# Kernel tuning notes

Hardware: AMD Instinct MI355X
Metric: run time of the kernel (lower is better)

Reference implementation:

```python
import jax, jax.numpy as jnp
import numpy as np

NEG_INF = -jnp.inf


def conv2d(x, w, b, stride, pad):
    # x: [B,C,H,W], w: [O,I,kh,kw]
    y = jax.lax.conv_general_dilated(
        x, w, window_strides=(stride, stride),
        padding=[(pad, pad), (pad, pad)],
        dimension_numbers=('NCHW', 'OIHW', 'NCHW'))
    return y + b[None, :, None, None]


def maxpool3s2(x):
    return jax.lax.reduce_window(x, -jnp.inf, jax.lax.max,
                                 (1, 1, 3, 3), (1, 1, 2, 2), 'VALID')


def setup_inputs() -> dict:
    key = jax.random.key(0)
    ks = jax.random.split(key, 20)
    s = 0.02
    B, C, H, W = 64, 3, 224, 224
    D, HID, OUT, E = 9216, 288, 1000, 8   # feature_dim, hidden_dim, output_dim, n_experts
    GH = 72                               # gate hidden = hidden_dim // 4
    inp = {
        'x':   jax.random.normal(ks[0], (B, C, H, W), jnp.float32),
        'c1w': s * jax.random.normal(ks[1], (64, 3, 11, 11), jnp.float32),
        'c1b': jnp.zeros((64,), jnp.float32),
        'c2w': s * jax.random.normal(ks[2], (192, 64, 5, 5), jnp.float32),
        'c2b': jnp.zeros((192,), jnp.float32),
        'c3w': s * jax.random.normal(ks[3], (384, 192, 3, 3), jnp.float32),
        'c3b': jnp.zeros((384,), jnp.float32),
        'c4w': s * jax.random.normal(ks[4], (256, 384, 3, 3), jnp.float32),
        'c4b': jnp.zeros((256,), jnp.float32),
        'c5w': s * jax.random.normal(ks[5], (256, 256, 3, 3), jnp.float32),
        'c5b': jnp.zeros((256,), jnp.float32),
        'gw1': s * jax.random.normal(ks[6], (D, GH), jnp.float32),
        'gb1': jnp.zeros((GH,), jnp.float32),
        'gw2': s * jax.random.normal(ks[7], (GH, E), jnp.float32),
        'gb2': jnp.zeros((E,), jnp.float32),
        'ew1': s * jax.random.normal(ks[8], (E, D, HID), jnp.float32),
        'eb1': jnp.zeros((E, HID), jnp.float32),
        'ew2': s * jax.random.normal(ks[9], (E, HID, HID // 2), jnp.float32),
        'eb2': jnp.zeros((E, HID // 2), jnp.float32),
        'ew3': s * jax.random.normal(ks[10], (E, HID // 2, OUT), jnp.float32),
        'eb3': jnp.zeros((E, OUT), jnp.float32),
    }
    return inp


def reference(x, c1w, c1b, c2w, c2b, c3w, c3b, c4w, c4b, c5w, c5b,
              gw1, gb1, gw2, gb2, ew1, eb1, ew2, eb2, ew3, eb3):
    # ---- AlexNet-style feature extractor (224 branch) ----
    h = jax.nn.relu(conv2d(x, c1w, c1b, 4, 2))   # [B,64,55,55]
    h = maxpool3s2(h)                             # [B,64,27,27]
    h = jax.nn.relu(conv2d(h, c2w, c2b, 1, 2))   # [B,192,27,27]
    h = maxpool3s2(h)                             # [B,192,13,13]
    h = jax.nn.relu(conv2d(h, c3w, c3b, 1, 1))   # [B,384,13,13]
    h = jax.nn.relu(conv2d(h, c4w, c4b, 1, 1))   # [B,256,13,13]
    h = jax.nn.relu(conv2d(h, c5w, c5b, 1, 1))   # [B,256,13,13]
    h = maxpool3s2(h)                             # [B,256,6,6]
    # AdaptiveAvgPool2d((6,6)) on a 6x6 input is the identity.
    feat = h.reshape(h.shape[0], -1)              # [B,9216]

    # ---- Gate: top-2 routing (eval mode: no noise, no dropout) ----
    g = jax.nn.relu(feat @ gw1 + gb1)             # [B,72]
    logits = g @ gw2 + gb2                        # [B,8]
    topv, topi = jax.lax.top_k(logits, 2)         # [B,2]
    topw = jax.nn.softmax(topv, axis=-1)          # softmax over top-2 only
    B = logits.shape[0]
    gates = jnp.zeros_like(logits).at[jnp.arange(B)[:, None], topi].set(topw)  # [B,8]

    # ---- Dense per-expert 3-layer MLP over full batch (as in source) ----
    h1 = jax.nn.relu(jnp.einsum('bd,edh->ebh', feat, ew1) + eb1[:, None, :])   # [E,B,288]
    h2 = jax.nn.relu(jnp.einsum('ebh,ehk->ebk', h1, ew2) + eb2[:, None, :])    # [E,B,144]
    eo = jnp.einsum('ebk,eko->ebo', h2, ew3) + eb3[:, None, :]                 # [E,B,1000]
    # Weighted combine; gates are zero for non-top-2 experts, matching the
    # masked accumulation loop in the torch forward.
    out = jnp.einsum('ebo,be->bo', eo, gates)     # [B,1000]
    return out
```

## Files before the change

kernel.cpp:

```cpp
#include <hip/hip_runtime.h>
#include <math.h>

#define TPB 256

typedef short s16x8 __attribute__((ext_vector_type(8)));
typedef short s16x4 __attribute__((ext_vector_type(4)));
typedef float f32x4 __attribute__((ext_vector_type(4)));

__device__ inline void bsplit(float x, short& h, short& l){
  union { float f; unsigned u; } a, hf, rf;
  a.f = x;
  unsigned hu = (a.u + 0x7FFFu + ((a.u >> 16) & 1u)) >> 16;
  h = (short)hu;
  hf.u = hu << 16;
  rf.f = x - hf.f;
  l = (short)((rf.u + 0x7FFFu + ((rf.u >> 16) & 1u)) >> 16);
}
__device__ inline float b2f(short s){
  union { unsigned u; float f; } x;
  x.u = ((unsigned)(unsigned short)s) << 16;
  return x.f;
}

__global__ __launch_bounds__(TPB) void wsplit_k(
    const float* __restrict__ w, short* __restrict__ wh, short* __restrict__ wl,
    int C, int O, int ntap, int total)
{
  int idx = blockIdx.x*TPB + threadIdx.x;
  if (idx >= total) return;
  int c   = idx % C;
  int t2  = idx / C;
  int oc  = t2 % O;
  int tap = t2 / O;
  float x = w[((size_t)oc*C + c)*ntap + tap];
  short h, l; bsplit(x, h, l);
  int tile = oc >> 4, ln = oc & 15;
  int S    = ntap*(C >> 5);
  int sl   = tap*(C >> 5) + (c >> 5);
  int lg   = (c >> 3) & 3, j = c & 7;
  size_t dst = (((size_t)tile*S + sl)*64 + lg*16 + ln)*8 + j;
  wh[dst] = h; wl[dst] = l;
}

__global__ __launch_bounds__(TPB) void wsplit1_k(
    const float* __restrict__ w, short* __restrict__ wh, short* __restrict__ wl)
{
  int idx = blockIdx.x*TPB + threadIdx.x;
  if (idx >= 64*576) return;
  int k  = idx % 576;
  int oc = idx / 576;
  int g  = k >> 4, kw = k & 15;
  int c  = g / 12, kh = g % 12;
  float x = 0.f;
  if (kh < 11 && kw < 11)
    x = w[((size_t)oc*3 + c)*121 + kh*11 + kw];
  short h, l; bsplit(x, h, l);
  int m = oc >> 4, ln = oc & 15;
  int s = k >> 5, r = k & 31;
  int lg = r >> 3, j = r & 7;
  size_t dst = (((size_t)m*18 + s)*64 + lg*16 + ln)*8 + j;
  wh[dst] = h; wl[dst] = l;
}

__global__ __launch_bounds__(TPB) void wtrans_k(
    const float* __restrict__ w, float* __restrict__ wT, int K, int O)
{
  int idx = blockIdx.x*TPB + threadIdx.x;
  if (idx >= K*O) return;
  int oc = idx % O;
  int k  = idx / O;
  wT[idx] = w[(size_t)oc*K + k];
}

#define C1W 240
#define CV1_PL 33
__global__ __launch_bounds__(256, 2) void conv1m_k(
    const float* __restrict__ in, const short* __restrict__ whi,
    const short* __restrict__ wlo, const float* __restrict__ bias,
    short* __restrict__ yh, short* __restrict__ yl)
{
  __shared__ __align__(16) short lds[2][CV1_PL*C1W + 84];
  const int tid = threadIdx.x;
  const int oh = blockIdx.x % 55;
  const int b  = blockIdx.x / 55;
  const int nt = tid >> 6;
  const int ln = tid & 15;
  const int lg = (tid & 63) >> 4;
  const int lane = tid & 63;
  const int ow = nt*16 + ln;

  const float* ip = in + (size_t)b*3*224*224;
  for (int i = tid; i < CV1_PL*59; i += 256){
    int plane = i / 59;
    int p     = i % 59;
    int c = plane / 11, kh = plane % 11;
    int ih = oh*4 - 2 + kh;
    int col0 = p*4;
    const float* rowp = (ih >= 0 && ih < 224) ? ip + (size_t)c*50176 + (size_t)ih*224 : nullptr;
    short h[4], l[4];
    #pragma unroll
    for (int j=0;j<4;++j){
      int iw = col0 + j - 2;
      float v = (rowp && iw >= 0 && iw < 224) ? rowp[iw] : 0.f;
      bsplit(v, h[j], l[j]);
    }
    s16x4 hv = {h[0],h[1],h[2],h[3]}, lv = {l[0],l[1],l[2],l[3]};
    *reinterpret_cast<s16x4*>(&lds[0][plane*C1W + col0]) = hv;
    *reinterpret_cast<s16x4*>(&lds[1][plane*C1W + col0]) = lv;
  }
  __syncthreads();

  f32x4 acc[4];
  #pragma unroll
  for (int m=0;m<4;++m){
    const float4 bv = *reinterpret_cast<const float4*>(bias + m*16 + lg*4);
    acc[m] = (f32x4){bv.x, bv.y, bv.z, bv.w};
  }

  s16x8 ah[4], al[4], ahn[4], aln[4];
  #pragma unroll
  for (int m=0;m<4;++m){
    size_t ao = (((size_t)m*18 + 0)*64 + lane)*8;
    ah[m] = *reinterpret_cast<const s16x8*>(whi + ao);
    al[m] = *reinterpret_cast<const s16x8*>(wlo + ao);
  }

  #pragma unroll 1
  for (int s=0; s<18; ++s){
    if (s < 17){
      #pragma unroll
      for (int m=0;m<4;++m){
        size_t ao = (((size_t)m*18 + s + 1)*64 + lane)*8;
        ahn[m] = *reinterpret_cast<const s16x8*>(whi + ao);
        aln[m] = *reinterpret_cast<const s16x8*>(wlo + ao);
      }
    }
    int g  = 2*s + (lg >> 1);
    int c  = g / 12, kh = g % 12;
    int plane = c*11 + (kh < 11 ? kh : 10);
    int base  = plane*C1W + ow*4 + (lg & 1)*8;
    s16x4 h0 = *reinterpret_cast<const s16x4*>(&lds[0][base]);
    s16x4 h1 = *reinterpret_cast<const s16x4*>(&lds[0][base+4]);
    s16x4 l0 = *reinterpret_cast<const s16x4*>(&lds[1][base]);
    s16x4 l1 = *reinterpret_cast<const s16x4*>(&lds[1][base+4]);
    s16x8 bh = __builtin_shufflevector(h0, h1, 0,1,2,3,4,5,6,7);
    s16x8 bl = __builtin_shufflevector(l0, l1, 0,1,2,3,4,5,6,7);
    #pragma unroll
    for (int m=0;m<4;++m){
      acc[m] = __builtin_amdgcn_mfma_f32_16x16x32_bf16(al[m], bh, acc[m], 0,0,0);
      acc[m] = __builtin_amdgcn_mfma_f32_16x16x32_bf16(ah[m], bl, acc[m], 0,0,0);
      acc[m] = __builtin_amdgcn_mfma_f32_16x16x32_bf16(ah[m], bh, acc[m], 0,0,0);
    }
    #pragma unroll
    for (int m=0;m<4;++m){ ah[m] = ahn[m]; al[m] = aln[m]; }
  }

  if (ow < 55){
    size_t base = ((size_t)b*3025 + (size_t)oh*55 + ow)*64;
    #pragma unroll
    for (int m=0;m<4;++m){
      short h[4], l[4];
      #pragma unroll
      for (int r=0;r<4;++r) bsplit(fmaxf(acc[m][r], 0.f), h[r], l[r]);
      s16x4 hv = {h[0],h[1],h[2],h[3]}, lv = {l[0],l[1],l[2],l[3]};
      *reinterpret_cast<s16x4*>(yh + base + m*16 + lg*4) = hv;
      *reinterpret_cast<s16x4*>(yl + base + m*16 + lg*4) = lv;
    }
  }
}

__global__ __launch_bounds__(TPB) void pool1_k(
    const short* __restrict__ xh, const short* __restrict__ xl,
    short* __restrict__ yh, short* __restrict__ yl)
{
  int i = blockIdx.x*TPB + threadIdx.x;
  if (i >= 64*729*64) return;
  int c = i & 63;
  int t = i >> 6;
  int sp = t % 729;
  int b = t / 729;
  int r = sp/27, cc = sp%27;
  const short* ph = xh + (size_t)b*3025*64 + c;
  const short* pl = xl + (size_t)b*3025*64 + c;
  float m = -INFINITY;
  #pragma unroll
  for (int di=0;di<3;++di)
    #pragma unroll
    for (int dj=0;dj<3;++dj){
      size_t s = (size_t)((2*r+di)*55 + 2*cc+dj)*64;
      m = fmaxf(m, b2f(ph[s]) + b2f(pl[s]));
    }
  short h, l; bsplit(m, h, l);
  yh[i] = h; yl[i] = l;
}

__global__ __launch_bounds__(256, 2) void conv2m_k(
    const short* __restrict__ xh, const short* __restrict__ xl,
    const short* __restrict__ whi, const short* __restrict__ wlo,
    const float* __restrict__ bias, short* __restrict__ yh, short* __restrict__ yl)
{
  __shared__ __align__(16) short lds[2][217*72];
  const int tid = threadIdx.x;
  const int rg  = blockIdx.x;
  const int b   = blockIdx.y;
  const int wid = tid >> 6;
  const int ln  = tid & 15;
  const int lg  = (tid & 63) >> 4;
  const int lane = tid & 63;
  const int oc0 = wid*48;
  const int r0  = rg*3;

  int sb[6], nn[6];
  #pragma unroll
  for (int t=0;t<6;++t){
    int n = t*16 + ln;
    nn[t] = n;
    int ohl = n / 27, ow = n % 27;
    sb[t] = (n < 81) ? (ohl*31 + ow) : 0;
  }

  f32x4 acc[3][6];
  #pragma unroll
  for (int m=0;m<3;++m){
    const float4 bv = *reinterpret_cast<const float4*>(bias + oc0 + m*16 + lg*4);
    #pragma unroll
    for (int t=0;t<6;++t) acc[m][t] = (f32x4){bv.x, bv.y, bv.z, bv.w};
  }

  for (int i = tid; i < 217*8; i += 256){
    int sp = i >> 3, v = i & 7;
    int pr = sp/31, pc = sp%31;
    int ih = r0 - 2 + pr, iw = pc - 2;
    s16x8 hv = {0,0,0,0,0,0,0,0}, lv = {0,0,0,0,0,0,0,0};
    if (ih >= 0 && ih < 27 && iw >= 0 && iw < 27){
      size_t o = ((size_t)b*729 + ih*27 + iw)*64 + v*8;
      hv = *reinterpret_cast<const s16x8*>(xh + o);
      lv = *reinterpret_cast<const s16x8*>(xl + o);
    }
    *reinterpret_cast<s16x8*>(&lds[0][sp*72 + v*8]) = hv;
    *reinterpret_cast<s16x8*>(&lds[1][sp*72 + v*8]) = lv;
  }
  __syncthreads();

  #pragma unroll 1
  for (int tap=0; tap<25; ++tap){
    const int toff = (tap/5)*31 + (tap%5);
    #pragma unroll
    for (int h2=0; h2<2; ++h2){
      const size_t wo = (((size_t)(wid*3)*50 + tap*2 + h2)*64 + lane)*8;
      s16x8 ah0 = *reinterpret_cast<const s16x8*>(whi + wo);
      s16x8 ah1 = *reinterpret_cast<const s16x8*>(whi + wo + 25600);
      s16x8 ah2 = *reinterpret_cast<const s16x8*>(whi + wo + 51200);
      s16x8 al0 = *reinterpret_cast<const s16x8*>(wlo + wo);
      s16x8 al1 = *reinterpret_cast<const s16x8*>(wlo + wo + 25600);
      s16x8 al2 = *reinterpret_cast<const s16x8*>(wlo + wo + 51200);
      #pragma unroll
      for (int t=0;t<6;++t){
        int off = (sb[t] + toff)*72 + h2*32 + lg*8;
        s16x8 bh = *reinterpret_cast<const s16x8*>(&lds[0][off]);
        s16x8 bl = *reinterpret_cast<const s16x8*>(&lds[1][off]);
        acc[0][t] = __builtin_amdgcn_mfma_f32_16x16x32_bf16(al0, bh, acc[0][t], 0,0,0);
        acc[0][t] = __builtin_amdgcn_mfma_f32_16x16x32_bf16(ah0, bl, acc[0][t], 0,0,0);
        acc[0][t] = __builtin_amdgcn_mfma_f32_16x16x32_bf16(ah0, bh, acc[0][t], 0,0,0);
        acc[1][t] = __builtin_amdgcn_mfma_f32_16x16x32_bf16(al1, bh, acc[1][t], 0,0,0);
        acc[1][t] = __builtin_amdgcn_mfma_f32_16x16x32_bf16(ah1, bl, acc[1][t], 0,0,0);
        acc[1][t] = __builtin_amdgcn_mfma_f32_16x16x32_bf16(ah1, bh, acc[1][t], 0,0,0);
        acc[2][t] = __builtin_amdgcn_mfma_f32_16x16x32_bf16(al2, bh, acc[2][t], 0,0,0);
        acc[2][t] = __builtin_amdgcn_mfma_f32_16x16x32_bf16(ah2, bl, acc[2][t], 0,0,0);
        acc[2][t] = __builtin_amdgcn_mfma_f32_16x16x32_bf16(ah2, bh, acc[2][t], 0,0,0);
      }
    }
  }

  #pragma unroll
  for (int m=0;m<3;++m)
    #pragma unroll
    for (int t=0;t<6;++t){
      if (nn[t] < 81){
        int gsp = r0*27 + nn[t];
        size_t base = ((size_t)b*729 + gsp)*192 + oc0 + m*16 + lg*4;
        short h[4], l[4];
        #pragma unroll
        for (int r=0;r<4;++r) bsplit(fmaxf(acc[m][t][r], 0.f), h[r], l[r]);
        s16x4 hv = {h[0],h[1],h[2],h[3]}, lv = {l[0],l[1],l[2],l[3]};
        *reinterpret_cast<s16x4*>(yh + base) = hv;
        *reinterpret_cast<s16x4*>(yl + base) = lv;
      }
    }
}

__global__ __launch_bounds__(TPB) void pool2_k(
    const short* __restrict__ xh, const short* __restrict__ xl,
    short* __restrict__ yh, short* __restrict__ yl)
{
  int i = blockIdx.x*TPB + threadIdx.x;
  if (i >= 64*169*192) return;
  int c = i % 192;
  int t = i / 192;
  int sp = t % 169;
  int b = t / 169;
  int r = sp/13, cc = sp%13;
  const short* ph = xh + (size_t)b*729*192 + c;
  const short* pl = xl + (size_t)b*729*192 + c;
  float m = -INFINITY;
  #pragma unroll
  for (int di=0;di<3;++di)
    #pragma unroll
    for (int dj=0;dj<3;++dj){
      size_t s = (size_t)((2*r+di)*27 + 2*cc+dj)*192;
      m = fmaxf(m, b2f(ph[s]) + b2f(pl[s]));
    }
  short h, l; bsplit(m, h, l);
  yh[i] = h; yl[i] = l;
}

template<int C,int O>
__global__ __launch_bounds__(256, 3) void conv3m_k(
    const short* __restrict__ xh, const short* __restrict__ xl,
    const short* __restrict__ whi, const short* __restrict__ wlo,
    const float* __restrict__ bias, short* __restrict__ yh, short* __restrict__ yl)
{
  __shared__ __align__(16) short lds[2][225*40];
  const int tid = threadIdx.x;
  const int b   = blockIdx.y;
  const int wid = tid >> 6;
  const int ln  = tid & 15;
  const int lg  = (tid & 63) >> 4;
  const int lane = tid & 63;
  const int tileIdx = blockIdx.x*2 + (wid & 1);
  const int oc0 = tileIdx*16;
  const int ng  = wid >> 1;
  const int tbase  = ng ? 6 : 0;
  const int ntiles = ng ? 5 : 6;
  const int S3 = 9*(C/32);

  int sb[6], nn[6];
  #pragma unroll
  for (int t=0;t<6;++t){
    int n = (tbase + t)*16 + ln;
    nn[t] = n;
    int oh = n / 13, ow = n % 13;
    sb[t] = (n < 169) ? (oh*15 + ow) : 0;
  }

  f32x4 acc[6];
  const float4 bv = *reinterpret_cast<const float4*>(bias + oc0 + lg*4);
  #pragma unroll
  for (int t=0;t<6;++t) acc[t] = (f32x4){bv.x, bv.y, bv.z, bv.w};

  #pragma unroll 1
  for (int c0=0; c0<C; c0+=32){
    __syncthreads();
    for (int i = tid; i < 225*4; i += 256){
      int sp = i >> 2, v = i & 3;
      int r = sp/15, cc = sp%15;
      s16x8 hv = {0,0,0,0,0,0,0,0}, lv = {0,0,0,0,0,0,0,0};
      if (r >= 1 && r <= 13 && cc >= 1 && cc <= 13){
        size_t o = ((size_t)b*169 + (r-1)*13 + (cc-1))*C + c0 + v*8;
        hv = *reinterpret_cast<const s16x8*>(xh + o);
        lv = *reinterpret_cast<const s16x8*>(xl + o);
      }
      *reinterpret_cast<s16x8*>(&lds[0][sp*40 + v*8]) = hv;
      *reinterpret_cast<s16x8*>(&lds[1][sp*40 + v*8]) = lv;
    }
    __syncthreads();

    const size_t tb = (size_t)tileIdx*S3 + (c0 >> 5);
    s16x8 ah = *reinterpret_cast<const s16x8*>(whi + (tb*64 + lane)*8);
    s16x8 al = *reinterpret_cast<const s16x8*>(wlo + (tb*64 + lane)*8);
    #pragma unroll 1
    for (int tap=0; tap<9; ++tap){
      s16x8 ahn = ah, aln = al;
      if (tap < 8){
        size_t ao = ((tb + (size_t)(tap+1)*(C/32))*64 + lane)*8;
        ahn = *reinterpret_cast<const s16x8*>(whi + ao);
        aln = *reinterpret_cast<const s16x8*>(wlo + ao);
      }
      const int toff = (tap/3)*15 + (tap%3);
      #pragma unroll
      for (int t=0;t<6;++t){
        if (t < ntiles){
          int off = (sb[t] + toff)*40 + lg*8;
          s16x8 bh = *reinterpret_cast<const s16x8*>(&lds[0][off]);
          s16x8 bl = *reinterpret_cast<const s16x8*>(&lds[1][off]);
          acc[t] = __builtin_amdgcn_mfma_f32_16x16x32_bf16(al, bh, acc[t], 0,0,0);
          acc[t] = __builtin_amdgcn_mfma_f32_16x16x32_bf16(ah, bl, acc[t], 0,0,0);
          acc[t] = __builtin_amdgcn_mfma_f32_16x16x32_bf16(ah, bh, acc[t], 0,0,0);
        }
      }
      ah = ahn; al = aln;
    }
  }

  #pragma unroll
  for (int t=0;t<6;++t){
    if (t < ntiles && nn[t] < 169){
      size_t base = ((size_t)b*169 + nn[t])*O + oc0 + lg*4;
      short h[4], l[4];
      #pragma unroll
      for (int r=0;r<4;++r) bsplit(fmaxf(acc[t][r], 0.f), h[r], l[r]);
      s16x4 hv = {h[0],h[1],h[2],h[3]}, lv = {l[0],l[1],l[2],l[3]};
      *reinterpret_cast<s16x4*>(yh + base) = hv;
      *reinterpret_cast<s16x4*>(yl + base) = lv;
    }
  }
}

__global__ __launch_bounds__(TPB) void pool3_k(
    const short* __restrict__ xh, const short* __restrict__ xl,
    float* __restrict__ feat)
{
  int i = blockIdx.x*TPB + threadIdx.x;
  if (i >= 64*9216) return;
  int d = i % 9216;
  int b = i / 9216;
  int c = d / 36;
  int sp = d % 36;
  int r = sp/6, cc = sp%6;
  const short* ph = xh + (size_t)b*169*256 + c;
  const short* pl = xl + (size_t)b*169*256 + c;
  float m = -INFINITY;
  #pragma unroll
  for (int di=0;di<3;++di)
    #pragma unroll
    for (int dj=0;dj<3;++dj){
      size_t s = (size_t)((2*r+di)*13 + 2*cc+dj)*256;
      m = fmaxf(m, b2f(ph[s]) + b2f(pl[s]));
    }
  feat[i] = m;
}

__global__ __launch_bounds__(256) void gate1_k(
    const float* __restrict__ feat, const float* __restrict__ gw1T,
    const float* __restrict__ gb1, float* __restrict__ g)
{
  const int b    = blockIdx.x;
  const int h    = blockIdx.y*4 + (threadIdx.x >> 6);
  const int lane = threadIdx.x & 63;
  const float* f = feat + (size_t)b*9216;
  const float* w = gw1T + (size_t)h*9216;
  float s = 0.f;
  #pragma unroll
  for (int it=0; it<36; ++it){
    int d = it*256 + lane*4;
    float4 fv = *reinterpret_cast<const float4*>(f + d);
    float4 wv = *reinterpret_cast<const float4*>(w + d);
    s = fmaf(fv.x, wv.x, s);
    s = fmaf(fv.y, wv.y, s);
    s = fmaf(fv.z, wv.z, s);
    s = fmaf(fv.w, wv.w, s);
  }
  #pragma unroll
  for (int off=32; off; off>>=1) s += __shfl_down(s, off, 64);
  if (lane == 0) g[(size_t)b*72 + h] = fmaxf(s + gb1[h], 0.f);
}

__global__ __launch_bounds__(128) void gate2_k(
    const float* __restrict__ g, const float* __restrict__ gw2,
    const float* __restrict__ gb2, float* __restrict__ gates)
{
  const int b = blockIdx.x;
  const int tid = threadIdx.x;
  __shared__ float gs[72];
  __shared__ float logits[8];
  if (tid < 72) gs[tid] = g[(size_t)b*72 + tid];
  __syncthreads();
  if (tid < 8) {
    float acc = gb2[tid];
    for (int j=0;j<72;++j)
      acc = fmaf(gs[j], gw2[(size_t)j*8 + tid], acc);
    logits[tid] = acc;
  }
  __syncthreads();
  if (tid == 0) {
    int i1 = 0; float v1 = logits[0];
    for (int e=1;e<8;++e) if (logits[e] > v1) { v1 = logits[e]; i1 = e; }
    int i2 = -1; float v2 = -INFINITY;
    for (int e=0;e<8;++e) { if (e==i1) continue; if (logits[e] > v2) { v2 = logits[e]; i2 = e; } }
    float z  = expf(v2 - v1);
    float w1 = 1.f / (1.f + z);
    float w2 = z   / (1.f + z);
    float* gr = gates + (size_t)b*8;
    for (int e=0;e<8;++e) gr[e] = 0.f;
    gr[i1] = w1;
    gr[i2] = w2;
  }
}

__global__ __launch_bounds__(256, 2) void eh1_part_k(
    const float* __restrict__ feat, const float* __restrict__ ew1,
    float* __restrict__ part)
{
  const int e  = blockIdx.x;
  const int ks = blockIdx.y;
  const int nb = blockIdx.z;
  const int h0 = nb*144;
  __shared__ __align__(16) float fs[64*33];
  __shared__ __align__(16) float wsh[32*144];
  const int tid = threadIdx.x;
  const int tx = tid & 15;
  const int ty = tid >> 4;
  float acc[4][9];
  #pragma unroll
  for (int i=0;i<4;++i)
    #pragma unroll
    for (int j=0;j<9;++j) acc[i][j]=0.f;
  const float* wbase = ew1 + (size_t)e*9216*288 + h0;
  for (int d0 = ks*192; d0 < ks*192+192; d0 += 32){
    __syncthreads();
    for (int l = tid; l < 512; l += 256){
      int r = l >> 3, c = l & 7;
      float4 v = *reinterpret_cast<const float4*>(feat + (size_t)r*9216 + d0 + c*4);
      float* dst = &fs[r*33 + c*4];
      dst[0]=v.x; dst[1]=v.y; dst[2]=v.z; dst[3]=v.w;
    }
    for (int l = tid; l < 1152; l += 256){
      int r = l / 36, c = l % 36;
      *reinterpret_cast<float4*>(&wsh[r*144 + c*4]) =
        *reinterpret_cast<const float4*>(wbase + (size_t)(d0 + r)*288 + c*4);
    }
    __syncthreads();
    #pragma unroll
    for (int k=0;k<32;++k){
      float fv[4], wv[9];
      #pragma unroll
      for (int i=0;i<4;++i) fv[i] = fs[(ty*4+i)*33 + k];
      #pragma unroll
      for (int j=0;j<9;++j) wv[j] = wsh[k*144 + tx*9 + j];
      #pragma unroll
      for (int i=0;i<4;++i)
        #pragma unroll
        for (int j=0;j<9;++j)
          acc[i][j] = fmaf(fv[i], wv[j], acc[i][j]);
    }
  }
  float* pp = part + (size_t)(ks*8 + e)*64*288;
  #pragma unroll
  for (int i=0;i<4;++i)
    #pragma unroll
    for (int j=0;j<9;++j)
      pp[(ty*4+i)*288 + h0 + tx*9 + j] = acc[i][j];
}

__global__ __launch_bounds__(TPB) void eh1_reduce_k(
    const float* __restrict__ part, const float* __restrict__ eb1,
    float* __restrict__ h1)
{
  int idx = blockIdx.x*TPB + threadIdx.x;
  if (idx >= 8*64*288) return;
  int h = idx % 288;
  int e = idx / (64*288);
  float a = eb1[(size_t)e*288 + h];
  #pragma unroll
  for (int s=0;s<48;++s)
    a += part[(size_t)s*147456 + idx];
  h1[idx] = fmaxf(a, 0.f);
}

__global__ __launch_bounds__(TPB) void expert_h2_k(
    const float* __restrict__ h1, const float* __restrict__ ew2,
    const float* __restrict__ eb2, const float* __restrict__ gates,
    float* __restrict__ h2)
{
  int idx = blockIdx.x*TPB + threadIdx.x;
  if (idx >= 8*64*144) return;
  int k = idx % 144;
  int t = idx / 144;
  int b = t % 64;
  int e = t / 64;
  if (gates[(size_t)b*8 + e] == 0.f) return;
  float acc = eb2[(size_t)e*144 + k];
  const float* h = h1 + ((size_t)e*64 + b)*288;
  const float* w = ew2 + (size_t)e*288*144 + k;
  for (int d=0; d<288; ++d)
    acc = fmaf(h[d], w[(size_t)d*144], acc);
  h2[idx] = fmaxf(acc, 0.f);
}

__global__ __launch_bounds__(TPB) void expert_out_k(
    const float* __restrict__ h2, const float* __restrict__ ew3,
    const float* __restrict__ eb3, const float* __restrict__ gates,
    float* __restrict__ out)
{
  int idx = blockIdx.x*TPB + threadIdx.x;
  if (idx >= 64*1000) return;
  int o = idx % 1000;
  int b = idx / 1000;
  float acc = 0.f;
  const float* gr = gates + (size_t)b*8;
  for (int e=0;e<8;++e){
    float ge = gr[e];
    if (ge == 0.f) continue;
    float a = eb3[(size_t)e*1000 + o];
    const float* h = h2 + ((size_t)e*64 + b)*144;
    const float* w = ew3 + (size_t)e*144*1000 + o;
    for (int k=0;k<144;++k)
      a = fmaf(h[k], w[(size_t)k*1000], a);
    acc = fmaf(ge, a, acc);
  }
  out[idx] = acc;
}

static inline int nblk(long long n){ return (int)((n + TPB - 1) / TPB); }

extern "C" void kernel_launch(void* const* d_in, const int* in_sizes, int n_in,
                              void* d_out, int out_size, void* d_ws, size_t ws_size,
                              hipStream_t stream)
{
  const float* x   = (const float*)d_in[0];
  const float* c1w = (const float*)d_in[1];  const float* c1b = (const float*)d_in[2];
  const float* c2w = (const float*)d_in[3];  const float* c2b = (const float*)d_in[4];
  const float* c3w = (const float*)d_in[5];  const float* c3b = (const float*)d_in[6];
  const float* c4w = (const float*)d_in[7];  const float* c4b = (const float*)d_in[8];
  const float* c5w = (const float*)d_in[9];  const float* c5b = (const float*)d_in[10];
  const float* gw1 = (const float*)d_in[11]; const float* gb1 = (const float*)d_in[12];
  const float* gw2 = (const float*)d_in[13]; const float* gb2 = (const float*)d_in[14];
  const float* ew1 = (const float*)d_in[15]; const float* eb1 = (const float*)d_in[16];
  const float* ew2 = (const float*)d_in[17]; const float* eb2 = (const float*)d_in[18];
  const float* ew3 = (const float*)d_in[19]; const float* eb3 = (const float*)d_in[20];
  float* out = (float*)d_out;

  float* W = (float*)d_ws;
  short* X1H = (short*)W;
  short* X1L = X1H + 12390400;
  short* X3H = (short*)W;
  short* X3L = X3H + 8957952;
  short* X5H = (short*)W;
  short* X5L = X5H + 4153344;
  short* X7H = (short*)W;
  short* X7L = X7H + 2768896;
  float* feat  = W + 5000000;
  float* part  = W + 6000000;
  short* WH2 = (short*)(W +  9000000);
  short* WL2 = WH2 + 307200;
  short* WH3 = (short*)(W +  9320000);
  short* WL3 = WH3 + 663552;
  short* WH4 = (short*)(W + 10000000);
  short* WL4 = WH4 + 884736;
  short* WH5 = (short*)(W + 10900000);
  short* WL5 = WH5 + 589824;
  float* GT1 = W + 11500000;
  short* X2H = (short*)(W + 12390400);
  short* X2L = X2H + 2985984;
  short* X4H = (short*)(W + 12390400);
  short* X4L = X4H + 2076672;
  short* X6H = (short*)(W + 12390400);
  short* X6L = X6H + 2768896;
  float* gates = W + 14000000;
  float* h1    = gates + 512;
  float* h2    = h1 + 147456;
  float* gbuf  = h2 + 73728;
  short* WH1 = (short*)(W + 15400000);
  short* WL1 = WH1 + 36864;
  (void)ws_size; (void)in_sizes; (void)n_in; (void)out_size;

  wsplit1_k<<<nblk(64LL*576), TPB, 0, stream>>>(c1w, WH1, WL1);
  conv1m_k<<<55*64, 256, 0, stream>>>(x, WH1, WL1, c1b, X1H, X1L);
  pool1_k<<<nblk(64LL*729*64), TPB, 0, stream>>>(X1H, X1L, X2H, X2L);
  wsplit_k<<<nblk(25LL*192*64),  TPB, 0, stream>>>(c2w, WH2, WL2,  64, 192, 25, 25*192*64);
  wsplit_k<<<nblk(9LL*384*192),  TPB, 0, stream>>>(c3w, WH3, WL3, 192, 384,  9, 9*384*192);
  wsplit_k<<<nblk(9LL*256*384),  TPB, 0, stream>>>(c4w, WH4, WL4, 384, 256,  9, 9*256*384);
  wsplit_k<<<nblk(9LL*256*256),  TPB, 0, stream>>>(c5w, WH5, WL5, 256, 256,  9, 9*256*256);
  wtrans_k<<<nblk(72LL*9216),    TPB, 0, stream>>>(gw1, GT1, 72, 9216);

  conv2m_k<<<dim3(9,64), 256, 0, stream>>>(X2H, X2L, WH2, WL2, c2b, X3H, X3L);
  pool2_k<<<nblk(64LL*169*192), TPB, 0, stream>>>(X3H, X3L, X4H, X4L);
  conv3m_k<192,384><<<dim3(12,64), 256, 0, stream>>>(X4H, X4L, WH3, WL3, c3b, X5H, X5L);
  conv3m_k<384,256><<<dim3(8,64),  256, 0, stream>>>(X5H, X5L, WH4, WL4, c4b, X6H, X6L);
  conv3m_k<256,256><<<dim3(8,64),  256, 0, stream>>>(X6H, X6L, WH5, WL5, c5b, X7H, X7L);
  pool3_k<<<nblk(64LL*9216), TPB, 0, stream>>>(X7H, X7L, feat);

  gate1_k<<<dim3(64,18), 256, 0, stream>>>(feat, GT1, gb1, gbuf);
  gate2_k<<<64, 128, 0, stream>>>(gbuf, gw2, gb2, gates);

  eh1_part_k<<<dim3(8,48,2), 256, 0, stream>>>(feat, ew1, part);
  eh1_reduce_k<<<nblk(8LL*64*288), TPB, 0, stream>>>(part, eb1, h1);
  expert_h2_k<<<nblk(8LL*64*144), TPB, 0, stream>>>(h1, ew2, eb2, gates, h2);
  expert_out_k<<<nblk(64LL*1000), TPB, 0, stream>>>(h2, ew3, eb3, gates, out);
}
```

Before: 610.3 us.

## Split conv2 input channels into halves to shrink LDS and prefetch weights

```diff
diff --git a/kernel.cpp b/kernel.cpp
--- a/kernel.cpp
+++ b/kernel.cpp
@@ -194,12 +194,12 @@
   yh[i] = h; yl[i] = l;
 }
 
-__global__ __launch_bounds__(256, 2) void conv2m_k(
+__global__ __launch_bounds__(256, 3) void conv2m_k(
     const short* __restrict__ xh, const short* __restrict__ xl,
     const short* __restrict__ whi, const short* __restrict__ wlo,
     const float* __restrict__ bias, short* __restrict__ yh, short* __restrict__ yl)
 {
-  __shared__ __align__(16) short lds[2][217*72];
+  __shared__ __align__(16) short lds[2][217*40];
   const int tid = threadIdx.x;
   const int rg  = blockIdx.x;
   const int b   = blockIdx.y;
@@ -227,36 +227,49 @@
     for (int t=0;t<6;++t) acc[m][t] = (f32x4){bv.x, bv.y, bv.z, bv.w};
   }
 
-  for (int i = tid; i < 217*8; i += 256){
-    int sp = i >> 3, v = i & 7;
-    int pr = sp/31, pc = sp%31;
-    int ih = r0 - 2 + pr, iw = pc - 2;
-    s16x8 hv = {0,0,0,0,0,0,0,0}, lv = {0,0,0,0,0,0,0,0};
-    if (ih >= 0 && ih < 27 && iw >= 0 && iw < 27){
-      size_t o = ((size_t)b*729 + ih*27 + iw)*64 + v*8;
-      hv = *reinterpret_cast<const s16x8*>(xh + o);
-      lv = *reinterpret_cast<const s16x8*>(xl + o);
-    }
-    *reinterpret_cast<s16x8*>(&lds[0][sp*72 + v*8]) = hv;
-    *reinterpret_cast<s16x8*>(&lds[1][sp*72 + v*8]) = lv;
-  }
-  __syncthreads();
-
   #pragma unroll 1
-  for (int tap=0; tap<25; ++tap){
-    const int toff = (tap/5)*31 + (tap%5);
-    #pragma unroll
-    for (int h2=0; h2<2; ++h2){
-      const size_t wo = (((size_t)(wid*3)*50 + tap*2 + h2)*64 + lane)*8;
-      s16x8 ah0 = *reinterpret_cast<const s16x8*>(whi + wo);
-      s16x8 ah1 = *reinterpret_cast<const s16x8*>(whi + wo + 25600);
-      s16x8 ah2 = *reinterpret_cast<const s16x8*>(whi + wo + 51200);
-      s16x8 al0 = *reinterpret_cast<const s16x8*>(wlo + wo);
-      s16x8 al1 = *reinterpret_cast<const s16x8*>(wlo + wo + 25600);
-      s16x8 al2 = *reinterpret_cast<const s16x8*>(wlo + wo + 51200);
+  for (int c0=0; c0<64; c0+=32){
+    __syncthreads();
+    for (int i = tid; i < 217*4; i += 256){
+      int sp = i >> 2, v = i & 3;
+      int pr = sp/31, pc = sp%31;
+      int ih = r0 - 2 + pr, iw = pc - 2;
+      s16x8 hv = {0,0,0,0,0,0,0,0}, lv = {0,0,0,0,0,0,0,0};
+      if (ih >= 0 && ih < 27 && iw >= 0 && iw < 27){
+        size_t o = ((size_t)b*729 + ih*27 + iw)*64 + c0 + v*8;
+        hv = *reinterpret_cast<const s16x8*>(xh + o);
+        lv = *reinterpret_cast<const s16x8*>(xl + o);
+      }
+      *reinterpret_cast<s16x8*>(&lds[0][sp*40 + v*8]) = hv;
+      *reinterpret_cast<s16x8*>(&lds[1][sp*40 + v*8]) = lv;
+    }
+    __syncthreads();
+
+    const size_t tstr = 50*512;
+    const size_t abase = ((size_t)(wid*3)*50 + (c0 >> 5))*512 + (size_t)lane*8;
+    s16x8 ah0 = *reinterpret_cast<const s16x8*>(whi + abase);
+    s16x8 ah1 = *reinterpret_cast<const s16x8*>(whi + abase + tstr);
+    s16x8 ah2 = *reinterpret_cast<const s16x8*>(whi + abase + 2*tstr);
+    s16x8 al0 = *reinterpret_cast<const s16x8*>(wlo + abase);
+    s16x8 al1 = *reinterpret_cast<const s16x8*>(wlo + abase + tstr);
+    s16x8 al2 = *reinterpret_cast<const s16x8*>(wlo + abase + 2*tstr);
+
+    #pragma unroll 1
+    for (int tap=0; tap<25; ++tap){
+      s16x8 nh0=ah0, nh1=ah1, nh2=ah2, nl0=al0, nl1=al1, nl2=al2;
+      if (tap < 24){
+        size_t ao = abase + (size_t)(tap+1)*2*512;
+        nh0 = *reinterpret_cast<const s16x8*>(whi + ao);
+        nh1 = *reinterpret_cast<const s16x8*>(whi + ao + tstr);
+        nh2 = *reinterpret_cast<const s16x8*>(whi + ao + 2*tstr);
+        nl0 = *reinterpret_cast<const s16x8*>(wlo + ao);
+        nl1 = *reinterpret_cast<const s16x8*>(wlo + ao + tstr);
+        nl2 = *reinterpret_cast<const s16x8*>(wlo + ao + 2*tstr);
+      }
+      const int toff = (tap/5)*31 + (tap%5);
       #pragma unroll
       for (int t=0;t<6;++t){
-        int off = (sb[t] + toff)*72 + h2*32 + lg*8;
+        int off = (sb[t] + toff)*40 + lg*8;
         s16x8 bh = *reinterpret_cast<const s16x8*>(&lds[0][off]);
         s16x8 bl = *reinterpret_cast<const s16x8*>(&lds[1][off]);
         acc[0][t] = __builtin_amdgcn_mfma_f32_16x16x32_bf16(al0, bh, acc[0][t], 0,0,0);
@@ -269,6 +282,7 @@
         acc[2][t] = __builtin_amdgcn_mfma_f32_16x16x32_bf16(ah2, bl, acc[2][t], 0,0,0);
         acc[2][t] = __builtin_amdgcn_mfma_f32_16x16x32_bf16(ah2, bh, acc[2][t], 0,0,0);
       }
+      ah0=nh0; ah1=nh1; ah2=nh2; al0=nl0; al1=nl1; al2=nl2;
     }
   }
 
```

New measurement: 585.1 us. -4.1%, faster.
